# Kernel tuning notes

Measured on AMD Instinct MI355X. Metric: run time of the kernel, lower is better.

The kernel has to match this reference:

```python
import jax, jax.numpy as jnp
import numpy as np

B, S, D, H, DFF, V, C, L = 2, 2048, 512, 8, 2048, 32000, 2, 2
DK = D // H
SCALE = 1.0 / np.sqrt(DK)
ALPHA = 0.3
GAMMA = 1.0
LN_EPS = 1e-5


def setup_inputs() -> dict:
    key = jax.random.key(0)
    ks = jax.random.split(key, 20)
    n = lambda k, shape: (jax.random.normal(k, shape, dtype=jnp.float32) * 0.02)
    inp = {
        "tokens": jax.random.randint(ks[0], (B, S), 0, V, dtype=jnp.int32),
        "embed": n(ks[1], (V, D)),
        "Wqr": n(ks[2], (L, D, D)), "Wqi": n(ks[3], (L, D, D)),
        "Wkr": n(ks[4], (L, D, D)), "Wki": n(ks[5], (L, D, D)),
        "Wv": n(ks[6], (L, D, D)),
        "Wo": n(ks[7], (L, D, D)), "bo": jnp.zeros((L, D), jnp.float32),
        "W1": n(ks[8], (L, D, DFF)), "b1": jnp.zeros((L, DFF), jnp.float32),
        "W2": n(ks[9], (L, DFF, D)), "b2": jnp.zeros((L, D), jnp.float32),
        "g1": jnp.ones((L, D), jnp.float32), "be1": jnp.zeros((L, D), jnp.float32),
        "g2": jnp.ones((L, D), jnp.float32), "be2": jnp.zeros((L, D), jnp.float32),
        "head_w": n(ks[10], (D, C)), "head_b": jnp.zeros((C,), jnp.float32),
    }
    return inp


def _layer_norm(x, g, b):
    mu = jnp.mean(x, axis=-1, keepdims=True)
    var = jnp.mean(jnp.square(x - mu), axis=-1, keepdims=True)
    return (x - mu) * jax.lax.rsqrt(var + LN_EPS) * g + b


def _pos_imag():
    # ComplexEmbeddings: omega = 1/10000^(arange(0,D,2)/D); imag = gamma*sin(omega*pos) repeat_interleave(2)
    freqs = 1.0 / (10000.0 ** (jnp.arange(0, D, 2, dtype=jnp.float32) / D))
    pos = jnp.arange(S, dtype=jnp.float32)[:, None]
    return GAMMA * jnp.repeat(jnp.sin(pos * freqs[None, :]), 2, axis=-1)  # [S, D]


def _forward(tokens, embed, Wqr, Wqi, Wkr, Wki, Wv, Wo, bo, W1, b1, W2, b2,
             g1, be1, g2, be2, head_w, head_b):
    zr = embed[tokens]                                  # [B,S,D]
    zi = jnp.broadcast_to(_pos_imag()[None], zr.shape)  # [B,S,D]

    def layer(carry, p):
        zr, zi = carry
        (wqr, wqi, wkr, wki, wv, wo, bo_, w1, b1_, w2, b2_, g1_, be1_, g2_, be2_) = p
        # complex Q = (zr + i zi) @ (wqr + i wqi)
        qr = (zr @ wqr - zi @ wqi).reshape(B, S, H, DK)
        qi = (zi @ wqr + zr @ wqi).reshape(B, S, H, DK)
        kr = (zr @ wkr - zi @ wki).reshape(B, S, H, DK)
        ki = (zi @ wkr + zr @ wki).reshape(B, S, H, DK)
        v = (zr @ wv).reshape(B, S, H, DK)
        # scores = Q @ conj(K)^T * scale
        sr = jnp.einsum('bqhd,bkhd->bhqk', qr, kr) + jnp.einsum('bqhd,bkhd->bhqk', qi, ki)
        si = jnp.einsum('bqhd,bkhd->bhqk', qi, kr) - jnp.einsum('bqhd,bkhd->bhqk', qr, ki)
        sr = sr * SCALE
        si = si * SCALE
        # hybrid: (|s| + alpha * cos(angle(s))) / sqrt(d_k)
        mag = jnp.sqrt(sr * sr + si * si)
        safe = jnp.where(mag == 0, 1.0, mag)
        phase = jnp.where(mag == 0, 1.0, sr / safe)  # cos(angle(0)) = 1
        scores = (mag + ALPHA * phase) / np.sqrt(DK)
        probs = jax.nn.softmax(scores, axis=-1)
        ctx = jnp.einsum('bhqk,bkhd->bqhd', probs, v).reshape(B, S, D)
        h = ctx @ wo + bo_
        z1 = _layer_norm(zr + h, g1_, be1_)
        ff = jax.nn.relu(z1 @ w1 + b1_) @ w2 + b2_
        z2 = _layer_norm(z1 + ff, g2_, be2_)
        # layer output is real; subsequent layers see zero imaginary part
        return (z2, jnp.zeros_like(z2)), None

    params = (Wqr, Wqi, Wkr, Wki, Wv, Wo, bo, W1, b1, W2, b2, g1, be1, g2, be2)
    (zr, _), _ = jax.lax.scan(layer, (zr, zi), params)
    return zr @ head_w + head_b  # [B,S,C]


def reference(tokens, embed, Wqr, Wqi, Wkr, Wki, Wv, Wo, bo, W1, b1, W2, b2,
              g1, be1, g2, be2, head_w, head_b):
    return _forward(tokens, embed, Wqr, Wqi, Wkr, Wki, Wv, Wo, bo, W1, b1, W2, b2,
                    g1, be1, g2, be2, head_w, head_b)
```

## Files before the change

kernel.cpp:

```cpp
#include <hip/hip_runtime.h>

#define B_   2
#define S_   2048
#define D_   512
#define H_   8
#define DK_  64
#define DFF_ 2048
#define L_   2
#define BS_  (B_*S_)
#define NPROJ 2560

typedef __attribute__((ext_vector_type(8))) short bfrag;
typedef __attribute__((ext_vector_type(4))) float facc;
typedef __attribute__((ext_vector_type(16))) float facc16;
typedef __attribute__((ext_vector_type(4))) int i4v;

__device__ __forceinline__ unsigned short f2b(float f) {
  union { float f; unsigned int u; } c; c.f = f;
  unsigned int u = c.u;
  u += 0x7fffu + ((u >> 16) & 1);
  return (unsigned short)(u >> 16);
}

__device__ __forceinline__ float b2f(unsigned short u) {
  union { unsigned u; float f; } c; c.u = (unsigned)u << 16; return c.f;
}

__device__ __forceinline__ bfrag asb(i4v x) { union { i4v a; bfrag b; } u; u.a = x; return u.b; }

__device__ __forceinline__ bfrag bneg(bfrag x) {
  union { bfrag b; i4v a; } u; u.b = x;
  u.a.x ^= 0x80008000; u.a.y ^= 0x80008000; u.a.z ^= 0x80008000; u.a.w ^= 0x80008000;
  return u.b;
}

__device__ __forceinline__ void async_copy16(const void* g, void* l) {
  __builtin_amdgcn_global_load_lds((const __attribute__((address_space(1))) void*)g,
                                   (__attribute__((address_space(3))) void*)l,
                                   16, 0, 0);
}

__global__ __launch_bounds__(128) void embed_zi_kernel(const int* __restrict__ tokens,
                                                       const float* __restrict__ embed,
                                                       float* __restrict__ zr,
                                                       unsigned short* __restrict__ acat) {
  int row = blockIdx.x;
  int tok = tokens[row];
  float4 v = ((const float4*)(embed + (size_t)tok * D_))[threadIdx.x];
  ((float4*)(zr + (size_t)row * D_))[threadIdx.x] = v;
  ushort4 o; o.x = f2b(v.x); o.y = f2b(v.y); o.z = f2b(v.z); o.w = f2b(v.w);
  *(ushort4*)(acat + (size_t)row * 1024 + threadIdx.x * 4) = o;

  int s = row & (S_ - 1);
  int d0 = threadIdx.x * 4;
  const double LN1E4 = 9.210340371976184;
  #pragma unroll
  for (int t = 0; t < 4; ++t) {
    int d = d0 + t;
    int jj = d >> 1;
    double freq = exp(-((double)jj / 256.0) * LN1E4);
    float val = (float)sin((double)s * freq);
    acat[(size_t)row * 1024 + 512 + d] = f2b(val);
  }
}

__global__ __launch_bounds__(256) void wcat_all(const float* __restrict__ Wqr,
                                                const float* __restrict__ Wqi,
                                                const float* __restrict__ Wkr,
                                                const float* __restrict__ Wki,
                                                const float* __restrict__ Wv,
                                                unsigned short* __restrict__ dst0,
                                                unsigned short* __restrict__ dst1) {
  __shared__ float tile[64][68];
  const int l = blockIdx.z;
  const int KA = l ? 512 : 1024;
  const int k0 = blockIdx.y * 64;
  if (k0 >= KA) return;
  unsigned short* dst = l ? dst1 : dst0;
  const size_t woff = (size_t)l * D_ * D_;
  const float* wqr = Wqr + woff;
  const float* wqi = Wqi + woff;
  const float* wkr = Wkr + woff;
  const float* wki = Wki + woff;
  const float* wv  = Wv  + woff;

  const int tid = threadIdx.x;
  const int n0 = blockIdx.x * 64;
  const int p = n0 >> 9, nn0 = n0 & 511;
  const float* src;
  float sign = 1.f;
  bool zero = false;
  if (k0 < 512) {
    const float* tops[5] = {wqr, wqi, wkr, wki, wv};
    src = tops[p];
  } else {
    const float* bots[5] = {wqi, wqr, wki, wkr, nullptr};
    const float sg[5] = {-1.f, 1.f, -1.f, 1.f, 0.f};
    src = bots[p]; sign = sg[p]; zero = (p == 4);
  }
  const int kk0 = k0 & 511;
  #pragma unroll
  for (int i = 0; i < 4; ++i) {
    int lin = tid + i * 256;
    int row = lin >> 4, c4 = (lin & 15) * 4;
    float4 v = make_float4(0.f, 0.f, 0.f, 0.f);
    if (!zero) v = *(const float4*)(src + (size_t)(kk0 + row) * 512 + nn0 + c4);
    *(float4*)&tile[row][c4] = v;
  }
  __syncthreads();
  #pragma unroll
  for (int i = 0; i < 4; ++i) {
    int lin = tid + i * 256;
    int n = lin >> 4, kc4 = (lin & 15) * 4;
    ushort4 o;
    o.x = f2b(sign * tile[kc4 + 0][n]);
    o.y = f2b(sign * tile[kc4 + 1][n]);
    o.z = f2b(sign * tile[kc4 + 2][n]);
    o.w = f2b(sign * tile[kc4 + 3][n]);
    *(ushort4*)(dst + (size_t)(n0 + n) * KA + k0 + kc4) = o;
  }
}

__global__ __launch_bounds__(256) void wtr_all(const float* __restrict__ Wo,
                                               const float* __restrict__ W1,
                                               const float* __restrict__ W2,
                                               unsigned short* __restrict__ pwo,
                                               unsigned short* __restrict__ pw1,
                                               unsigned short* __restrict__ pw2) {
  __shared__ float tile[64][68];
  const int j = blockIdx.z, l = j & 1;
  const float* src; unsigned short* dst; int K, N;
  if (j < 2)      { src = Wo + (size_t)l * 512 * 512;  dst = pwo + (size_t)l * 512 * 512;  K = 512;  N = 512; }
  else if (j < 4) { src = W1 + (size_t)l * 512 * 2048; dst = pw1 + (size_t)l * 2048 * 512; K = 512;  N = 2048; }
  else            { src = W2 + (size_t)l * 2048 * 512; dst = pw2 + (size_t)l * 512 * 2048; K = 2048; N = 512; }
  const int n0 = blockIdx.x * 64, k0 = blockIdx.y * 64;
  if (n0 >= N || k0 >= K) return;
  const int tid = threadIdx.x;
  #pragma unroll
  for (int i = 0; i < 4; ++i) {
    int lin = tid + i * 256;
    int row = lin >> 4, c4 = (lin & 15) * 4;
    *(float4*)&tile[row][c4] = *(const float4*)(src + (size_t)(k0 + row) * N + n0 + c4);
  }
  __syncthreads();
  #pragma unroll
  for (int i = 0; i < 4; ++i) {
    int lin = tid + i * 256;
    int n = lin >> 4, kc4 = (lin & 15) * 4;
    ushort4 o;
    o.x = f2b(tile[kc4 + 0][n]);
    o.y = f2b(tile[kc4 + 1][n]);
    o.z = f2b(tile[kc4 + 2][n]);
    o.w = f2b(tile[kc4 + 3][n]);
    *(ushort4*)(dst + (size_t)(n0 + n) * K + k0 + kc4) = o;
  }
}

template<int TM, int TN>
__global__ __launch_bounds__(256) void gemm_bf16(const unsigned short* __restrict__ A,
                                                 const unsigned short* __restrict__ Bt,
                                                 const float* __restrict__ bias,
                                                 float* __restrict__ outF,
                                                 unsigned short* __restrict__ outB,
                                                 unsigned short* __restrict__ vt,
                                                 int M, int N, int K, int lda, int relu) {
  constexpr int MT = TM / 32;
  constexpr int NT = TN / 32;
  constexpr int NL = TM / 64 + TN / 64;
  __shared__ short smem[3 * (TM + TN) * 32];

  const int tid = threadIdx.x;
  const int w = tid >> 6, lane = tid & 63;
  const int col = lane & 15, quad = lane >> 4;

  const int nwg = gridDim.x * gridDim.y;
  const int bid = blockIdx.y * gridDim.x + blockIdx.x;
  const int cpx = nwg >> 3;
  const int swz = (bid & 7) * cpx + (bid >> 3);
  const int bx = swz % gridDim.x, by = swz / gridDim.x;

  const int m0 = by * TM, n0 = bx * TN;
  const int wrow = (w >> 1) * (TM / 2);
  const int wcol = (w & 1) * (TN / 2);

  const int srow = lane >> 2;
  const int skk  = (lane & 3) * 8;

  facc acc[MT][NT];
  #pragma unroll
  for (int i = 0; i < MT; ++i)
    #pragma unroll
    for (int j = 0; j < NT; ++j) acc[i][j] = (facc){0.f, 0.f, 0.f, 0.f};

  auto stage = [&](int k0, int buf) {
    short* A_s = smem + buf * (TM + TN) * 32;
    short* B_s = A_s + TM * 32;
    #pragma unroll
    for (int rd = 0; rd < TM / 64; ++rd) {
      int row = rd * 64 + w * 16 + srow;
      async_copy16(A + (size_t)(m0 + row) * lda + k0 + skk, &A_s[row * 32 + skk]);
    }
    #pragma unroll
    for (int rd = 0; rd < TN / 64; ++rd) {
      int row = rd * 64 + w * 16 + srow;
      async_copy16(Bt + (size_t)(n0 + row) * K + k0 + skk, &B_s[row * 32 + skk]);
    }
  };

  const int nT = K >> 5;
  stage(0, 0);
  if (nT > 1) stage(32, 1);

  int cur = 0;
  for (int t = 0; t < nT; ++t) {
    if (t + 2 < nT) {
      int nb = cur + 2; if (nb >= 3) nb -= 3;
      stage((t + 2) * 32, nb);
    }
    const int fut = (t + 1 < nT) + (t + 2 < nT);
    if constexpr (NL == 4) {
      if (fut == 2)      asm volatile("s_waitcnt vmcnt(8)" ::: "memory");
      else if (fut == 1) asm volatile("s_waitcnt vmcnt(4)" ::: "memory");
      else               asm volatile("s_waitcnt vmcnt(0)" ::: "memory");
    } else {
      if (fut == 2)      asm volatile("s_waitcnt vmcnt(4)" ::: "memory");
      else if (fut == 1) asm volatile("s_waitcnt vmcnt(2)" ::: "memory");
      else               asm volatile("s_waitcnt vmcnt(0)" ::: "memory");
    }
    __builtin_amdgcn_s_barrier();
    asm volatile("" ::: "memory");

    const short* A_s = smem + cur * (TM + TN) * 32;
    const short* B_s = A_s + TM * 32;

    bfrag af[MT], bf[NT];
    #pragma unroll
    for (int i = 0; i < MT; ++i)
      af[i] = *(const bfrag*)&A_s[(wrow + i * 16 + col) * 32 + quad * 8];
    #pragma unroll
    for (int j = 0; j < NT; ++j)
      bf[j] = *(const bfrag*)&B_s[(wcol + j * 16 + col) * 32 + quad * 8];
    #pragma unroll
    for (int i = 0; i < MT; ++i)
      #pragma unroll
      for (int j = 0; j < NT; ++j)
        acc[i][j] = __builtin_amdgcn_mfma_f32_16x16x32_bf16(af[i], bf[j], acc[i][j], 0, 0, 0);

    __builtin_amdgcn_s_barrier();
    asm volatile("" ::: "memory");
    cur = (cur == 2) ? 0 : cur + 1;
  }

  #pragma unroll
  for (int i = 0; i < MT; ++i) {
    #pragma unroll
    for (int j = 0; j < NT; ++j) {
      int colIdx = n0 + wcol + j * 16 + col;
      float b = bias ? bias[colIdx] : 0.f;
      int rowBase = m0 + wrow + i * 16 + quad * 4;
      if (vt && colIdx >= 2048) {
        int c = colIdx - 2048;
        int bh = ((rowBase >> 11) << 3) + (c >> 6);
        int d = c & 63;
        int s = rowBase & (S_ - 1);
        ushort4 o;
        o.x = f2b(acc[i][j][0]); o.y = f2b(acc[i][j][1]);
        o.z = f2b(acc[i][j][2]); o.w = f2b(acc[i][j][3]);
        *(ushort4*)(vt + ((size_t)bh * DK_ + d) * S_ + s) = o;
      } else {
        #pragma unroll
        for (int r = 0; r < 4; ++r) {
          int rowIdx = rowBase + r;
          float v = acc[i][j][r] + b;
          if (relu) v = fmaxf(v, 0.f);
          if (outF) outF[(size_t)rowIdx * N + colIdx] = v;
          if (outB) outB[(size_t)rowIdx * N + colIdx] = f2b(v);
        }
      }
    }
  }
}

__global__ __launch_bounds__(512, 2) void attn_mfma(const unsigned short* __restrict__ Q4,
                                                    const unsigned short* __restrict__ VT,
                                                    unsigned short* __restrict__ po,
                                                    float* __restrict__ pl) {
  __shared__ __align__(16) short smem[32768];

  const int bh = blockIdx.y;
  const int b = bh >> 3, hd = bh & 7;
  const int hoff = hd * DK_;
  const int ks = blockIdx.z;
  const int tid = threadIdx.x;
  const int w = tid >> 6;
  const int lane = tid & 63;
  const int m = lane & 31;
  const int h = lane >> 5;
  const int x7 = m & 7;
  const int q0 = blockIdx.x * 256 + w * 32;
  const int kb = ks * 512;

  const size_t bS = (size_t)b * S_;
  const size_t vtbase = (size_t)bh * DK_ * S_;

  const int skey = tid >> 3, sseg = tid & 7;
  const int sls = sseg ^ (skey & 7);

  bfrag qrf[4], qif[4], nqrf[4];
  {
    const size_t qrow = (bS + q0 + m) * (size_t)NPROJ + hoff;
    #pragma unroll
    for (int t = 0; t < 4; ++t) {
      qrf[t] = *(const bfrag*)(Q4 + qrow + t * 16 + h * 8);
      qif[t] = *(const bfrag*)(Q4 + qrow + 512 + t * 16 + h * 8);
      nqrf[t] = bneg(qrf[t]);
    }
  }

  facc16 o0 = {}, o1 = {};
  float l = 0.f;
  const float c1 = 0.015625f;
  const float c2 = 0.0375f;

  const unsigned short* vb0 = VT + vtbase + (size_t)m * S_ + kb + h * 8;
  const unsigned short* vb1 = vb0 + (size_t)32 * S_;

  char* kr_sb = (char*)smem;
  char* ki_sb = (char*)smem + 32768;

  for (int ph = 0; ph < 2; ++ph) {
    __builtin_amdgcn_s_barrier();
    #pragma unroll
    for (int r = 0; r < 4; ++r) {
      const unsigned short* gk = Q4 + (bS + kb + ph * 256 + r * 64 + skey) * (size_t)NPROJ
                               + 1024 + hoff + sls * 8;
      async_copy16(gk,       kr_sb + r * 8192 + tid * 16);
      async_copy16(gk + 512, ki_sb + r * 8192 + tid * 16);
    }
    asm volatile("s_waitcnt vmcnt(0)" ::: "memory");
    __builtin_amdgcn_s_barrier();
    asm volatile("" ::: "memory");

    for (int c = 0; c < 4; ++c) {
      bfrag vtf[2][4];
      #pragma unroll
      for (int kt = 0; kt < 4; ++kt) {
        vtf[0][kt] = *(const bfrag*)(vb0 + kt * 16);
        vtf[1][kt] = *(const bfrag*)(vb1 + kt * 16);
      }
      vb0 += 64; vb1 += 64;

      bfrag kr0[4], ki0[4], kr1[4], ki1[4];
      #pragma unroll
      for (int t = 0; t < 4; ++t) {
        int off0 = (c * 64 + m) * 128 + (((2 * t + h) ^ x7) << 4);
        int off1 = (c * 64 + 32 + m) * 128 + (((2 * t + h) ^ x7) << 4);
        kr0[t] = *(const bfrag*)(kr_sb + off0);
        ki0[t] = *(const bfrag*)(ki_sb + off0);
        kr1[t] = *(const bfrag*)(kr_sb + off1);
        ki1[t] = *(const bfrag*)(ki_sb + off1);
      }

      facc16 sr0 = {}, si0 = {}, sr1 = {}, si1 = {};
      #pragma unroll
      for (int t = 0; t < 4; ++t) {
        sr0 = __builtin_amdgcn_mfma_f32_32x32x16_bf16(kr0[t], qrf[t], sr0, 0, 0, 0);
        si0 = __builtin_amdgcn_mfma_f32_32x32x16_bf16(kr0[t], qif[t], si0, 0, 0, 0);
        sr0 = __builtin_amdgcn_mfma_f32_32x32x16_bf16(ki0[t], qif[t], sr0, 0, 0, 0);
        si0 = __builtin_amdgcn_mfma_f32_32x32x16_bf16(ki0[t], nqrf[t], si0, 0, 0, 0);
      }
      #pragma unroll
      for (int t = 0; t < 4; ++t) {
        sr1 = __builtin_amdgcn_mfma_f32_32x32x16_bf16(kr1[t], qrf[t], sr1, 0, 0, 0);
        si1 = __builtin_amdgcn_mfma_f32_32x32x16_bf16(kr1[t], qif[t], si1, 0, 0, 0);
        sr1 = __builtin_amdgcn_mfma_f32_32x32x16_bf16(ki1[t], qif[t], sr1, 0, 0, 0);
        si1 = __builtin_amdgcn_mfma_f32_32x32x16_bf16(ki1[t], nqrf[t], si1, 0, 0, 0);
      }

      #pragma unroll
      for (int hs = 0; hs < 2; ++hs) {
        const facc16& sr = hs ? sr1 : sr0;
        const facc16& si = hs ? si1 : si0;

        float p[16], ssum = 0.f;
        #pragma unroll
        for (int i = 0; i < 16; ++i) {
          float a = sr[i], bb = si[i];
          float d2 = __builtin_fmaf(a, a, __builtin_fmaf(bb, bb, 1e-30f));
          float rs = rsqrtf(d2);
          float x = rs * __builtin_fmaf(c1, d2, c2 * a);
          p[i] = __builtin_fmaf(x, __builtin_fmaf(0.5f, x, 1.f), 1.f);
          ssum += p[i];
        }
        l += ssum;

        unsigned dw[8];
        #pragma unroll
        for (int i = 0; i < 8; ++i)
          asm("v_cvt_pk_bf16_f32 %0, %1, %2" : "=v"(dw[i]) : "v"(p[2 * i]), "v"(p[2 * i + 1]));
        unsigned s0a = dw[0], s0b = dw[2];
        unsigned s1a = dw[1], s1b = dw[3];
        unsigned s2a = dw[4], s2b = dw[6];
        unsigned s3a = dw[5], s3b = dw[7];
        asm("v_permlane32_swap_b32 %0, %1" : "+v"(s0a), "+v"(s0b));
        asm("v_permlane32_swap_b32 %0, %1" : "+v"(s1a), "+v"(s1b));
        asm("v_permlane32_swap_b32 %0, %1" : "+v"(s2a), "+v"(s2b));
        asm("v_permlane32_swap_b32 %0, %1" : "+v"(s3a), "+v"(s3b));
        i4v f0 = { (int)s0a, (int)s1a, (int)s0b, (int)s1b };
        i4v f1 = { (int)s2a, (int)s3a, (int)s2b, (int)s3b };
        bfrag pf0 = asb(f0), pf1 = asb(f1);

        o0 = __builtin_amdgcn_mfma_f32_32x32x16_bf16(vtf[0][2 * hs + 0], pf0, o0, 0, 0, 0);
        o0 = __builtin_amdgcn_mfma_f32_32x32x16_bf16(vtf[0][2 * hs + 1], pf1, o0, 0, 0, 0);
        o1 = __builtin_amdgcn_mfma_f32_32x32x16_bf16(vtf[1][2 * hs + 0], pf0, o1, 0, 0, 0);
        o1 = __builtin_amdgcn_mfma_f32_32x32x16_bf16(vtf[1][2 * hs + 1], pf1, o1, 0, 0, 0);
      }
    }
  }

  float l_tot = l + __shfl_xor(l, 32);
  const size_t prow = ((size_t)(bh * 4 + ks)) * S_ + q0 + m;
  #pragma unroll
  for (int tile = 0; tile < 2; ++tile) {
    const facc16& oo = tile ? o1 : o0;
    #pragma unroll
    for (int rg = 0; rg < 4; ++rg) {
      int d0 = tile * 32 + rg * 8 + h * 4;
      ushort4 ob;
      ob.x = f2b(oo[4 * rg + 0]);
      ob.y = f2b(oo[4 * rg + 1]);
      ob.z = f2b(oo[4 * rg + 2]);
      ob.w = f2b(oo[4 * rg + 3]);
      *(ushort4*)(po + prow * 64 + d0) = ob;
    }
  }
  if (lane < 32) pl[prow] = l_tot;
}

__global__ __launch_bounds__(256) void attn_combine(const unsigned short* __restrict__ po,
                                                    const float* __restrict__ pl,
                                                    unsigned short* __restrict__ ctxb) {
  int t = blockIdx.x * 256 + threadIdx.x;
  int row = t >> 3;
  int dg = t & 7;
  int bh = row >> 11, q = row & (S_ - 1);
  int b = bh >> 3, hd = bh & 7;
  float acc[8];
  #pragma unroll
  for (int e = 0; e < 8; ++e) acc[e] = 0.f;
  float ls = 0.f;
  #pragma unroll
  for (int ks = 0; ks < 4; ++ks) {
    size_t prow = (((size_t)(bh * 4 + ks)) << 11) + q;
    ls += pl[prow];
    const unsigned short* src = po + prow * 64 + dg * 8;
    ushort4 v0 = *(const ushort4*)src;
    ushort4 v1 = *(const ushort4*)(src + 4);
    acc[0] += b2f(v0.x); acc[1] += b2f(v0.y); acc[2] += b2f(v0.z); acc[3] += b2f(v0.w);
    acc[4] += b2f(v1.x); acc[5] += b2f(v1.y); acc[6] += b2f(v1.z); acc[7] += b2f(v1.w);
  }
  float inv = 1.f / ls;
  unsigned short ob[8];
  #pragma unroll
  for (int e = 0; e < 8; ++e) ob[e] = f2b(acc[e] * inv);
  *(int4*)(ctxb + ((size_t)(b * S_ + q)) * D_ + hd * DK_ + dg * 8) = *(const int4*)ob;
}

__global__ __launch_bounds__(256) void ln_kernel(const float* __restrict__ X,
                                                 const float* __restrict__ R,
                                                 const float* __restrict__ g,
                                                 const float* __restrict__ be,
                                                 float* __restrict__ OutF,
                                                 unsigned short* __restrict__ OutB,
                                                 const float* __restrict__ hw,
                                                 const float* __restrict__ hb,
                                                 float* __restrict__ hout) {
  const int lane = threadIdx.x & 63;
  const int wv = threadIdx.x >> 6;
  const int row = blockIdx.x * 4 + wv;
  const float* xp = X + (size_t)row * D_;
  const float* rp = R + (size_t)row * D_;
  float x[8];
  float s = 0.f;
  #pragma unroll
  for (int i = 0; i < 8; ++i) {
    int d = i * 64 + lane;
    x[i] = xp[d] + rp[d];
    s += x[i];
  }
  s += __shfl_xor(s, 32); s += __shfl_xor(s, 16); s += __shfl_xor(s, 8);
  s += __shfl_xor(s, 4);  s += __shfl_xor(s, 2);  s += __shfl_xor(s, 1);
  float mu = s * (1.f / 512.f);
  float vs = 0.f;
  #pragma unroll
  for (int i = 0; i < 8; ++i) { float d = x[i] - mu; vs += d * d; }
  vs += __shfl_xor(vs, 32); vs += __shfl_xor(vs, 16); vs += __shfl_xor(vs, 8);
  vs += __shfl_xor(vs, 4);  vs += __shfl_xor(vs, 2);  vs += __shfl_xor(vs, 1);
  float rstd = rsqrtf(vs * (1.f / 512.f) + 1e-5f);
  float a0 = 0.f, a1 = 0.f;
  #pragma unroll
  for (int i = 0; i < 8; ++i) {
    int d = i * 64 + lane;
    float v = (x[i] - mu) * rstd * g[d] + be[d];
    if (OutF) OutF[(size_t)row * D_ + d] = v;
    if (OutB) OutB[(size_t)row * D_ + d] = f2b(v);
    if (hout) { a0 += v * hw[d * 2]; a1 += v * hw[d * 2 + 1]; }
  }
  if (hout) {
    a0 += __shfl_xor(a0, 32); a0 += __shfl_xor(a0, 16); a0 += __shfl_xor(a0, 8);
    a0 += __shfl_xor(a0, 4);  a0 += __shfl_xor(a0, 2);  a0 += __shfl_xor(a0, 1);
    a1 += __shfl_xor(a1, 32); a1 += __shfl_xor(a1, 16); a1 += __shfl_xor(a1, 8);
    a1 += __shfl_xor(a1, 4);  a1 += __shfl_xor(a1, 2);  a1 += __shfl_xor(a1, 1);
    if (lane == 0) {
      hout[row * 2]     = a0 + hb[0];
      hout[row * 2 + 1] = a1 + hb[1];
    }
  }
}

extern "C" void kernel_launch(void* const* d_in, const int* in_sizes, int n_in,
                              void* d_out, int out_size, void* d_ws, size_t ws_size,
                              hipStream_t stream) {
  const int*   tokens = (const int*)  d_in[0];
  const float* embed  = (const float*)d_in[1];
  const float* Wqr = (const float*)d_in[2];
  const float* Wqi = (const float*)d_in[3];
  const float* Wkr = (const float*)d_in[4];
  const float* Wki = (const float*)d_in[5];
  const float* Wv  = (const float*)d_in[6];
  const float* Wo  = (const float*)d_in[7];
  const float* bo  = (const float*)d_in[8];
  const float* W1  = (const float*)d_in[9];
  const float* b1  = (const float*)d_in[10];
  const float* W2  = (const float*)d_in[11];
  const float* b2  = (const float*)d_in[12];
  const float* g1  = (const float*)d_in[13];
  const float* be1 = (const float*)d_in[14];
  const float* g2  = (const float*)d_in[15];
  const float* be2 = (const float*)d_in[16];
  const float* hw  = (const float*)d_in[17];
  const float* hb  = (const float*)d_in[18];
  float* out = (float*)d_out;

  char* p = (char*)d_ws;
  float* zr = (float*)p;             p += (size_t)BS_ * D_ * 4;
  unsigned short* acat = (unsigned short*)p;
  unsigned short* zrb  = acat;       p += (size_t)BS_ * 1024 * 2;
  unsigned short* Q4   = (unsigned short*)p;
  unsigned short* ffb  = Q4;         p += (size_t)BS_ * NPROJ * 2;
  unsigned short* VT   = (unsigned short*)p; p += (size_t)B_*H_*DK_*S_*2;
  unsigned short* ctxb = (unsigned short*)p; p += (size_t)BS_ * D_ * 2;
  float* hbuf = (float*)p;           p += (size_t)BS_ * D_ * 4;
  float* z1   = (float*)p;           p += (size_t)BS_ * D_ * 4;
  unsigned short* z1b = (unsigned short*)p;  p += (size_t)BS_ * D_ * 2;
  unsigned short* pw_proj0 = (unsigned short*)p; p += (size_t)NPROJ * 1024 * 2;
  unsigned short* pw_proj1 = (unsigned short*)p; p += (size_t)NPROJ * 512 * 2;
  unsigned short* pw_wo = (unsigned short*)p;    p += (size_t)2 * 512 * 512 * 2;
  unsigned short* pw_w1 = (unsigned short*)p;    p += (size_t)2 * 2048 * 512 * 2;
  unsigned short* pw_w2 = (unsigned short*)p;    p += (size_t)2 * 512 * 2048 * 2;
  float* pl = (float*)p;             p += (size_t)16 * 4 * S_ * 4;

  unsigned short* po = (unsigned short*)hbuf;

  embed_zi_kernel<<<BS_, 128, 0, stream>>>(tokens, embed, zr, acat);
  wcat_all<<<dim3(NPROJ / 64, 16, 2), 256, 0, stream>>>(Wqr, Wqi, Wkr, Wki, Wv,
                                                        pw_proj0, pw_proj1);
  wtr_all<<<dim3(32, 32, 6), 256, 0, stream>>>(Wo, W1, W2, pw_wo, pw_w1, pw_w2);

  for (int l = 0; l < L_; ++l) {
    const int KA = (l == 0) ? 1024 : 512;
    const unsigned short* Aproj = (l == 0) ? acat : zrb;
    const unsigned short* Wproj = (l == 0) ? pw_proj0 : pw_proj1;

    gemm_bf16<128, 128><<<dim3(NPROJ / 128, BS_ / 128), 256, 0, stream>>>(
        Aproj, Wproj, nullptr, nullptr, Q4, VT, BS_, NPROJ, KA, KA, 0);

    attn_mfma<<<dim3(S_ / 256, B_ * H_, 4), 512, 0, stream>>>(Q4, VT, po, pl);
    attn_combine<<<1024, 256, 0, stream>>>(po, pl, ctxb);

    gemm_bf16<64, 64><<<dim3(D_ / 64, BS_ / 64), 256, 0, stream>>>(
        ctxb, pw_wo + (size_t)l * 512 * 512, bo + l * D_, hbuf, nullptr, nullptr,
        BS_, D_, D_, D_, 0);
    ln_kernel<<<BS_ / 4, 256, 0, stream>>>(zr, hbuf, g1 + l * D_, be1 + l * D_, z1, z1b,
                                           nullptr, nullptr, nullptr);

    gemm_bf16<128, 128><<<dim3(DFF_ / 128, BS_ / 128), 256, 0, stream>>>(
        z1b, pw_w1 + (size_t)l * 2048 * 512, b1 + l * DFF_, nullptr, ffb, nullptr,
        BS_, DFF_, D_, D_, 1);
    gemm_bf16<64, 64><<<dim3(D_ / 64, BS_ / 64), 256, 0, stream>>>(
        ffb, pw_w2 + (size_t)l * 512 * 2048, b2 + l * D_, hbuf, nullptr, nullptr,
        BS_, D_, DFF_, DFF_, 0);
    if (l == L_ - 1)
      ln_kernel<<<BS_ / 4, 256, 0, stream>>>(z1, hbuf, g2 + l * D_, be2 + l * D_,
                                             nullptr, nullptr, hw, hb, out);
    else
      ln_kernel<<<BS_ / 4, 256, 0, stream>>>(z1, hbuf, g2 + l * D_, be2 + l * D_,
                                             zr, zrb, nullptr, nullptr, nullptr);
  }
}
```

Before: 475.3 us.

## Split-K the N=512 GEMMs and fold partial reduction plus bias into LayerNorm

The Wo and W2 GEMMs now launch with a K-split of two, each slice writing its own fp32 partial output buffer without bias. The LayerNorm kernel sums both partials, the residual and the bias before normalizing. This raises the number of workgroups and shortens each block's K loop for these narrow-N GEMMs. In exchange it writes and reads an extra fp32 activation-sized buffer per GEMM.

Result: slower. 502.5 us (+5.7%).

```diff
diff --git a/kernel.cpp b/kernel.cpp
--- a/kernel.cpp
+++ b/kernel.cpp
@@ -183,6 +183,9 @@
   const int wrow = (w >> 1) * (TM / 2);
   const int wcol = (w & 1) * (TN / 2);
 
+  const int Klen = K / gridDim.z;
+  const int kbase = blockIdx.z * Klen;
+
   const int srow = lane >> 2;
   const int skk  = (lane & 3) * 8;
 
@@ -198,16 +201,16 @@
     #pragma unroll
     for (int rd = 0; rd < TM / 64; ++rd) {
       int row = rd * 64 + w * 16 + srow;
-      async_copy16(A + (size_t)(m0 + row) * lda + k0 + skk, &A_s[row * 32 + skk]);
+      async_copy16(A + (size_t)(m0 + row) * lda + kbase + k0 + skk, &A_s[row * 32 + skk]);
     }
     #pragma unroll
     for (int rd = 0; rd < TN / 64; ++rd) {
       int row = rd * 64 + w * 16 + srow;
-      async_copy16(Bt + (size_t)(n0 + row) * K + k0 + skk, &B_s[row * 32 + skk]);
+      async_copy16(Bt + (size_t)(n0 + row) * K + kbase + k0 + skk, &B_s[row * 32 + skk]);
     }
   };
 
-  const int nT = K >> 5;
+  const int nT = Klen >> 5;
   stage(0, 0);
   if (nT > 1) stage(32, 1);
 
@@ -250,6 +253,8 @@
     asm volatile("" ::: "memory");
     cur = (cur == 2) ? 0 : cur + 1;
   }
+
+  float* outFz = outF ? outF + (size_t)blockIdx.z * M * N : nullptr;
 
   #pragma unroll
   for (int i = 0; i < MT; ++i) {
@@ -273,7 +278,7 @@
           int rowIdx = rowBase + r;
           float v = acc[i][j][r] + b;
           if (relu) v = fmaxf(v, 0.f);
-          if (outF) outF[(size_t)rowIdx * N + colIdx] = v;
+          if (outFz) outFz[(size_t)rowIdx * N + colIdx] = v;
           if (outB) outB[(size_t)rowIdx * N + colIdx] = f2b(v);
         }
       }
@@ -468,6 +473,8 @@
 
 __global__ __launch_bounds__(256) void ln_kernel(const float* __restrict__ X,
                                                  const float* __restrict__ R,
+                                                 const float* __restrict__ R2,
+                                                 const float* __restrict__ gb,
                                                  const float* __restrict__ g,
                                                  const float* __restrict__ be,
                                                  float* __restrict__ OutF,
@@ -480,12 +487,13 @@
   const int row = blockIdx.x * 4 + wv;
   const float* xp = X + (size_t)row * D_;
   const float* rp = R + (size_t)row * D_;
+  const float* r2p = R2 + (size_t)row * D_;
   float x[8];
   float s = 0.f;
   #pragma unroll
   for (int i = 0; i < 8; ++i) {
     int d = i * 64 + lane;
-    x[i] = xp[d] + rp[d];
+    x[i] = xp[d] + rp[d] + r2p[d] + gb[d];
     s += x[i];
   }
   s += __shfl_xor(s, 32); s += __shfl_xor(s, 16); s += __shfl_xor(s, 8);
@@ -550,7 +558,7 @@
   unsigned short* ffb  = Q4;         p += (size_t)BS_ * NPROJ * 2;
   unsigned short* VT   = (unsigned short*)p; p += (size_t)B_*H_*DK_*S_*2;
   unsigned short* ctxb = (unsigned short*)p; p += (size_t)BS_ * D_ * 2;
-  float* hbuf = (float*)p;           p += (size_t)BS_ * D_ * 4;
+  float* hbuf = (float*)p;           p += (size_t)2 * BS_ * D_ * 4;
   float* z1   = (float*)p;           p += (size_t)BS_ * D_ * 4;
   unsigned short* z1b = (unsigned short*)p;  p += (size_t)BS_ * D_ * 2;
   unsigned short* pw_proj0 = (unsigned short*)p; p += (size_t)NPROJ * 1024 * 2;
@@ -578,23 +586,26 @@
     attn_mfma<<<dim3(S_ / 256, B_ * H_, 4), 512, 0, stream>>>(Q4, VT, po, pl);
     attn_combine<<<1024, 256, 0, stream>>>(po, pl, ctxb);
 
-    gemm_bf16<64, 64><<<dim3(D_ / 64, BS_ / 64), 256, 0, stream>>>(
-        ctxb, pw_wo + (size_t)l * 512 * 512, bo + l * D_, hbuf, nullptr, nullptr,
+    gemm_bf16<64, 64><<<dim3(D_ / 64, BS_ / 64, 2), 256, 0, stream>>>(
+        ctxb, pw_wo + (size_t)l * 512 * 512, nullptr, hbuf, nullptr, nullptr,
         BS_, D_, D_, D_, 0);
-    ln_kernel<<<BS_ / 4, 256, 0, stream>>>(zr, hbuf, g1 + l * D_, be1 + l * D_, z1, z1b,
-                                           nullptr, nullptr, nullptr);
+    ln_kernel<<<BS_ / 4, 256, 0, stream>>>(zr, hbuf, hbuf + (size_t)BS_ * D_,
+                                           bo + l * D_, g1 + l * D_, be1 + l * D_,
+                                           z1, z1b, nullptr, nullptr, nullptr);
 
     gemm_bf16<128, 128><<<dim3(DFF_ / 128, BS_ / 128), 256, 0, stream>>>(
         z1b, pw_w1 + (size_t)l * 2048 * 512, b1 + l * DFF_, nullptr, ffb, nullptr,
         BS_, DFF_, D_, D_, 1);
-    gemm_bf16<64, 64><<<dim3(D_ / 64, BS_ / 64), 256, 0, stream>>>(
-        ffb, pw_w2 + (size_t)l * 512 * 2048, b2 + l * D_, hbuf, nullptr, nullptr,
+    gemm_bf16<64, 64><<<dim3(D_ / 64, BS_ / 64, 2), 256, 0, stream>>>(
+        ffb, pw_w2 + (size_t)l * 512 * 2048, nullptr, hbuf, nullptr, nullptr,
         BS_, D_, DFF_, DFF_, 0);
     if (l == L_ - 1)
-      ln_kernel<<<BS_ / 4, 256, 0, stream>>>(z1, hbuf, g2 + l * D_, be2 + l * D_,
+      ln_kernel<<<BS_ / 4, 256, 0, stream>>>(z1, hbuf, hbuf + (size_t)BS_ * D_,
+                                             b2 + l * D_, g2 + l * D_, be2 + l * D_,
                                              nullptr, nullptr, hw, hb, out);
     else
-      ln_kernel<<<BS_ / 4, 256, 0, stream>>>(z1, hbuf, g2 + l * D_, be2 + l * D_,
+      ln_kernel<<<BS_ / 4, 256, 0, stream>>>(z1, hbuf, hbuf + (size_t)BS_ * D_,
+                                             b2 + l * D_, g2 + l * D_, be2 + l * D_,
                                              zr, zrb, nullptr, nullptr, nullptr);
   }
 }
```
